# Kernel optimization log

Hardware: AMD Instinct MI355X
Metric: run time of the kernel (lower is better)

## Reference

```python
import jax, jax.numpy as jnp
import numpy as np

TOP_K = 6  # num_experts_per_tok


def setup_inputs() -> dict:
    key = jax.random.key(0)
    k1, k2, k3, k4, k5 = jax.random.split(key, 5)
    B, S, H = 2, 2048, 2048
    E, M = 28, 1408
    scale = 0.02
    return {
        "hidden_states": jax.random.normal(k1, (B, S, H), jnp.float32),
        "gate_weight": jax.random.normal(k2, (E, H), jnp.float32) * scale,
        "w_gate": jax.random.normal(k3, (E, H, M), jnp.float32) * scale,
        "w_up": jax.random.normal(k4, (E, H, M), jnp.float32) * scale,
        "w_down": jax.random.normal(k5, (E, M, H), jnp.float32) * scale,
    }


def reference(hidden_states, gate_weight, w_gate, w_up, w_down):
    """DeepseekMoE forward (inference path): top-k softmax gating + expert
    dispatch/combine. gate_weight: [E, H]; w_gate/w_up: [E, H, M]; w_down: [E, M, H]."""
    B, S, H = hidden_states.shape
    x = hidden_states.reshape(-1, H)          # [T, H]
    T = x.shape[0]
    E = gate_weight.shape[0]

    # --- MoEGate: softmax scores, top-k, normalize top-k probs ---
    logits = x @ gate_weight.T                # [T, E]
    scores = jax.nn.softmax(logits, axis=-1)
    topk_w, topk_idx = jax.lax.top_k(scores, TOP_K)  # [T, K]
    topk_w = topk_w / (topk_w.sum(axis=-1, keepdims=True) + 1e-20)

    # Dense per-(token, expert) combine weights (0 for non-selected experts).
    cw = jnp.zeros((T, E), x.dtype).at[jnp.arange(T)[:, None], topk_idx].add(topk_w)

    # --- Expert compute + combine, scanning over experts to bound memory ---
    def step(y, inp):
        wg, wu, wd, w_tok = inp               # [H,M], [H,M], [M,H], [T]
        h = jax.nn.silu(x @ wg) * (x @ wu)    # [T, M]
        return y + w_tok[:, None] * (h @ wd), None

    y0 = jnp.zeros_like(x)
    y, _ = jax.lax.scan(step, y0, (w_gate, w_up, w_down, cw.T))
    return y.reshape(B, S, H)
```

## Files before the change

### kernel.cpp

```cpp
#include <hip/hip_runtime.h>
#include <stdint.h>

#define T_TOK 4096
#define HDIM 2048
#define MDIM 1408
#define NEXP 28
#define TOPK 6
#define NPAIR (T_TOK*TOPK)

typedef unsigned short u16;
typedef short short8 __attribute__((ext_vector_type(8)));
typedef float f32x4 __attribute__((ext_vector_type(4)));

__device__ __forceinline__ u16 f2bf(float x){
  unsigned int u = __float_as_uint(x);
  u += 0x7fffu + ((u >> 16) & 1u);
  return (u16)(u >> 16);
}

__device__ __forceinline__ void gload16(const u16* g, u16* l){
  __builtin_amdgcn_global_load_lds((const __attribute__((address_space(1))) unsigned int*)g,
                                   (__attribute__((address_space(3))) unsigned int*)l,
                                   16, 0, 0);
}

__global__ __launch_bounds__(256) void cvt_kernel(const float* __restrict__ x,
                                                  u16* __restrict__ xb, int n8){
  int i = blockIdx.x*256 + threadIdx.x;
  if (i >= n8) return;
  const float4* s = (const float4*)x + (size_t)i*2;
  float4 a = s[0], b = s[1];
  unsigned int w0 = (unsigned)f2bf(a.x) | ((unsigned)f2bf(a.y)<<16);
  unsigned int w1 = (unsigned)f2bf(a.z) | ((unsigned)f2bf(a.w)<<16);
  unsigned int w2 = (unsigned)f2bf(b.x) | ((unsigned)f2bf(b.y)<<16);
  unsigned int w3 = (unsigned)f2bf(b.z) | ((unsigned)f2bf(b.w)<<16);
  uint4 o = {w0,w1,w2,w3};
  ((uint4*)xb)[i] = o;
}

__global__ __launch_bounds__(256) void transpose_cvt(const float* __restrict__ in,
                                                     u16* __restrict__ out, int K, int N){
  const int e = blockIdx.z;
  const int n0 = blockIdx.x*64, k0 = blockIdx.y*64;
  const float* src = in + ((size_t)e*K + k0)*N + n0;
  u16* dst = out + ((size_t)e*N + n0)*K + k0;
  __shared__ u16 td[64][65];
  const int tid = threadIdx.x;
  const int rk = tid>>4, rn = (tid&15)*4;
  #pragma unroll
  for (int i=0;i<4;i++){
    int k = rk + 16*i;
    float4 v = *(const float4*)(src + (size_t)k*N + rn);
    td[k][rn+0]=f2bf(v.x); td[k][rn+1]=f2bf(v.y);
    td[k][rn+2]=f2bf(v.z); td[k][rn+3]=f2bf(v.w);
  }
  __syncthreads();
  const int wn = tid>>4, wk = (tid&15)*4;
  #pragma unroll
  for (int i=0;i<4;i++){
    int n = wn + 16*i;
    unsigned int lo = (unsigned)td[wk+0][n] | ((unsigned)td[wk+1][n]<<16);
    unsigned int hi = (unsigned)td[wk+2][n] | ((unsigned)td[wk+3][n]<<16);
    uint2 o = {lo, hi};
    *(uint2*)(dst + (size_t)n*K + wk) = o;
  }
}

__global__ __launch_bounds__(256) void gate_kernel(const float* __restrict__ x,
                                                   const float* __restrict__ gw,
                                                   int* __restrict__ topk_idx,
                                                   float* __restrict__ topk_w,
                                                   int* __restrict__ counts){
  const int wave = threadIdx.x >> 6, lane = threadIdx.x & 63;
  const int t = blockIdx.x*4 + wave;
  const float* xr = x + (size_t)t*HDIM;
  float xv[32];
  #pragma unroll
  for (int i=0;i<32;i++) xv[i] = xr[lane + 64*i];
  float sc[NEXP];
  #pragma unroll
  for (int e=0;e<NEXP;e++){
    const float* g = gw + (size_t)e*HDIM + lane;
    float a = 0.f;
    #pragma unroll
    for (int i=0;i<32;i++) a += xv[i]*g[64*i];
    #pragma unroll
    for (int d=32; d>0; d>>=1) a += __shfl_xor(a, d);
    sc[e] = a;
  }
  float mx = sc[0];
  #pragma unroll
  for (int e=1;e<NEXP;e++) mx = fmaxf(mx, sc[e]);
  unsigned int mask=0; int bi[TOPK]; float bs[TOPK]; float bsum=0.f;
  #pragma unroll
  for (int k=0;k<TOPK;k++){
    float bm=-3.4e38f; int bj=0;
    #pragma unroll
    for (int e=0;e<NEXP;e++){
      bool ok = (((mask>>e)&1u)==0u) && (sc[e]>bm);
      bm = ok ? sc[e] : bm; bj = ok ? e : bj;
    }
    mask |= (1u<<bj);
    float s = expf(bm - mx);
    bi[k]=bj; bs[k]=s; bsum+=s;
  }
  if (lane==0){
    float inv = 1.f/(bsum + 1e-20f);
    #pragma unroll
    for (int k=0;k<TOPK;k++){
      topk_idx[t*TOPK+k]=bi[k];
      topk_w[t*TOPK+k]=bs[k]*inv;
      atomicAdd(&counts[bi[k]],1);
    }
  }
}

__global__ void scan_kernel(const int* __restrict__ counts, int* __restrict__ offsets,
                            int* __restrict__ cursor){
  int t = threadIdx.x;
  if (t < NEXP) cursor[t] = 0;
  if (t == 0){
    int s = 0;
    for (int e=0;e<NEXP;e++){ offsets[e]=s; s+=counts[e]; }
    offsets[NEXP]=s;
  }
}

__global__ __launch_bounds__(256) void fill_kernel(const int* __restrict__ topk_idx,
                                                   const float* __restrict__ topk_w,
                                                   const int* __restrict__ offsets,
                                                   int* __restrict__ cursor,
                                                   int* __restrict__ pair_token,
                                                   float* __restrict__ pair_w){
  int t = blockIdx.x*256 + threadIdx.x;
  if (t >= T_TOK) return;
  #pragma unroll
  for (int k=0;k<TOPK;k++){
    int e = topk_idx[t*TOPK+k];
    int pos = atomicAdd(&cursor[e],1);
    int p = offsets[e]+pos;
    pair_token[p]=t;
    pair_w[p]=topk_w[t*TOPK+k];
  }
}

template<int NB, bool GATHER, int EPI>
__global__ __launch_bounds__(256,2) void gemm2(
    const u16* __restrict__ Ab, const u16* __restrict__ B0, const u16* __restrict__ B1,
    u16* __restrict__ Hout, float* __restrict__ Out,
    const int* __restrict__ counts, const int* __restrict__ offsets,
    const int* __restrict__ pair_token, const float* __restrict__ pair_w,
    int K, int N)
{
  const int e = blockIdx.z;
  const int cnt = counts[e];
  const int row0 = blockIdx.y*128;
  if (row0 >= cnt) return;
  const int off = offsets[e];
  const int n0 = blockIdx.x*128;

  __shared__ u16 smem[(1+NB)*8192];

  const int tid = threadIdx.x;
  const int lane = tid&63, wid = tid>>6;
  const int wm = wid>>1, wn = wid&1;
  const int lrow = lane&15, lgrp = lane>>4;

  const u16* ap[4]; const u16* bp0[4]; const u16* bp1[4];
  #pragma unroll
  for (int i=0;i<4;i++){
    int c = tid + 256*i;
    int r = c>>3;
    int sc = (c&7) ^ (r&7);
    int pr = off + min(row0 + r, cnt-1);
    const u16* arow = GATHER ? (Ab + (size_t)pair_token[pr]*K) : (Ab + (size_t)pr*K);
    ap[i] = arow + sc*8;
    size_t brow = (size_t)e*N + (size_t)(n0 + r);
    bp0[i] = B0 + brow*K + sc*8;
    if (NB==2) bp1[i] = B1 + brow*K + sc*8;
  }

  int aoffs[2][4], boffs[2][4];
  #pragma unroll
  for (int kh=0;kh<2;kh++){
    #pragma unroll
    for (int f=0; f<4; f++){
      int mr = wm*64 + f*16 + lrow;
      aoffs[kh][f] = mr*64 + (((kh*4+lgrp) ^ (mr&7))*8);
      int nr = wn*64 + f*16 + lrow;
      boffs[kh][f] = nr*64 + (((kh*4+lgrp) ^ (nr&7))*8);
    }
  }

  f32x4 acc0[4][4] = {};
  f32x4 acc1[4][4] = {};

  for (int kt=0; kt<K; kt+=64){
    __syncthreads();
    #pragma unroll
    for (int i=0;i<4;i++){
      int ldo = (tid + 256*i)*8;
      gload16(ap[i] + kt, &smem[ldo]);
      gload16(bp0[i] + kt, &smem[8192 + ldo]);
      if (NB==2) gload16(bp1[i] + kt, &smem[16384 + ldo]);
    }
    __syncthreads();
    #pragma unroll
    for (int kh=0; kh<2; kh++){
      short8 af[4], b0f[4], b1f[4];
      #pragma unroll
      for (int f=0;f<4;f++){
        af[f]  = *(const short8*)&smem[aoffs[kh][f]];
        b0f[f] = *(const short8*)&smem[8192 + boffs[kh][f]];
        if (NB==2) b1f[f] = *(const short8*)&smem[16384 + boffs[kh][f]];
      }
      #pragma unroll
      for (int fm=0;fm<4;fm++){
        #pragma unroll
        for (int fn=0;fn<4;fn++){
          acc0[fm][fn] = __builtin_amdgcn_mfma_f32_16x16x32_bf16(af[fm], b0f[fn], acc0[fm][fn],0,0,0);
          if (NB==2)
            acc1[fm][fn] = __builtin_amdgcn_mfma_f32_16x16x32_bf16(af[fm], b1f[fn], acc1[fm][fn],0,0,0);
        }
      }
    }
  }

  #pragma unroll
  for (int fm=0;fm<4;fm++){
    #pragma unroll
    for (int j=0;j<4;j++){
      int grow = wm*64 + fm*16 + lgrp*4 + j;
      if (row0+grow < cnt){
        int p = off + row0 + grow;
        if (EPI==0){
          u16* hrow = Hout + (size_t)p*N;
          #pragma unroll
          for (int fn=0;fn<4;fn++){
            int col = n0 + wn*64 + fn*16 + lrow;
            float g = acc0[fm][fn][j], u = acc1[fm][fn][j];
            hrow[col] = f2bf(g*u/(1.f+expf(-g)));
          }
        } else {
          int tok = pair_token[p];
          float wgt = pair_w[p];
          float* orow = Out + (size_t)tok*N;
          #pragma unroll
          for (int fn=0;fn<4;fn++){
            int col = n0 + wn*64 + fn*16 + lrow;
            atomicAdd(orow + col, wgt*acc0[fm][fn][j]);
          }
        }
      }
    }
  }
}

extern "C" void kernel_launch(void* const* d_in, const int* in_sizes, int n_in,
                              void* d_out, int out_size, void* d_ws, size_t ws_size,
                              hipStream_t stream) {
  const float* x  = (const float*)d_in[0];
  const float* gw = (const float*)d_in[1];
  const float* wg = (const float*)d_in[2];
  const float* wu = (const float*)d_in[3];
  const float* wd = (const float*)d_in[4];
  float* out = (float*)d_out;

  const size_t WT_BYTES = (size_t)NEXP*MDIM*HDIM*2;

  char* p = (char*)d_ws;
  u16* wg_t = (u16*)p;
  u16* wd_t = (u16*)p;
  p += WT_BYTES;
  u16* wu_t = (u16*)p; p += WT_BYTES;
  u16* xb   = (u16*)p; p += (size_t)T_TOK*HDIM*2;
  u16* hbuf = (u16*)p; p += (size_t)NPAIR*MDIM*2;
  int*   topk_idx   = (int*)p;   p += NPAIR*4;
  float* topk_w     = (float*)p; p += NPAIR*4;
  int*   pair_token = (int*)p;   p += NPAIR*4;
  float* pair_w     = (float*)p; p += NPAIR*4;
  int*   counts     = (int*)p;   p += 128;
  int*   offsets    = (int*)p;   p += 128;
  int*   cursor     = (int*)p;   p += 128;

  hipMemsetAsync(counts, 0, 128, stream);
  cvt_kernel<<<T_TOK*HDIM/8/256, 256, 0, stream>>>(x, xb, T_TOK*HDIM/8);
  gate_kernel<<<T_TOK/4, 256, 0, stream>>>(x, gw, topk_idx, topk_w, counts);
  scan_kernel<<<1, 64, 0, stream>>>(counts, offsets, cursor);
  fill_kernel<<<T_TOK/256, 256, 0, stream>>>(topk_idx, topk_w, offsets, cursor, pair_token, pair_w);
  hipMemsetAsync(out, 0, (size_t)out_size*4, stream);

  transpose_cvt<<<dim3(MDIM/64, HDIM/64, NEXP), 256, 0, stream>>>(wg, wg_t, HDIM, MDIM);
  transpose_cvt<<<dim3(MDIM/64, HDIM/64, NEXP), 256, 0, stream>>>(wu, wu_t, HDIM, MDIM);

  gemm2<2,true,0><<<dim3(MDIM/128, T_TOK/128, NEXP), 256, 0, stream>>>(
      xb, wg_t, wu_t, hbuf, nullptr, counts, offsets, pair_token, pair_w, HDIM, MDIM);

  transpose_cvt<<<dim3(HDIM/64, MDIM/64, NEXP), 256, 0, stream>>>(wd, wd_t, MDIM, HDIM);

  gemm2<1,false,1><<<dim3(HDIM/128, T_TOK/128, NEXP), 256, 0, stream>>>(
      hbuf, wd_t, nullptr, nullptr, out, counts, offsets, pair_token, pair_w, MDIM, HDIM);
}
```

Baseline: 1.212 ms.

## Double-buffer MoE GEMM K-loop, replace atomic combine with gather kernel

Restructures the grouped expert GEMM to use BK=32 with double-buffered LDS, issuing the next tile's async global-to-LDS loads before waiting with explicit vmcnt, so memory latency overlaps MFMA work. The grid order is swapped so row tiles are the fastest-varying block index. The down-projection no longer does float atomicAdd into the output. It writes bf16 per-pair results, and a new combine kernel gathers the six pairs per token with their weights, which also drops the output memset. It also widens the transpose store to 16-byte writes with padded LDS. The costs are an extra bf16 rounding of the down-projection outputs and a second pass over a per-pair buffer.

Result: slower. 2.484 ms (+105.0%).

```diff
diff --git a/kernel.cpp b/kernel.cpp
--- a/kernel.cpp
+++ b/kernel.cpp
@@ -16,6 +16,9 @@
   unsigned int u = __float_as_uint(x);
   u += 0x7fffu + ((u >> 16) & 1u);
   return (u16)(u >> 16);
+}
+__device__ __forceinline__ float bf2f(unsigned int h){
+  return __uint_as_float(h << 16);
 }
 
 __device__ __forceinline__ void gload16(const u16* g, u16* l){
@@ -44,7 +47,7 @@
   const int n0 = blockIdx.x*64, k0 = blockIdx.y*64;
   const float* src = in + ((size_t)e*K + k0)*N + n0;
   u16* dst = out + ((size_t)e*N + n0)*K + k0;
-  __shared__ u16 td[64][65];
+  __shared__ u16 td[64][72];
   const int tid = threadIdx.x;
   const int rk = tid>>4, rn = (tid&15)*4;
   #pragma unroll
@@ -55,14 +58,16 @@
     td[k][rn+2]=f2bf(v.z); td[k][rn+3]=f2bf(v.w);
   }
   __syncthreads();
-  const int wn = tid>>4, wk = (tid&15)*4;
-  #pragma unroll
-  for (int i=0;i<4;i++){
-    int n = wn + 16*i;
-    unsigned int lo = (unsigned)td[wk+0][n] | ((unsigned)td[wk+1][n]<<16);
-    unsigned int hi = (unsigned)td[wk+2][n] | ((unsigned)td[wk+3][n]<<16);
-    uint2 o = {lo, hi};
-    *(uint2*)(dst + (size_t)n*K + wk) = o;
+  const int k8 = (tid&7)*8;
+  #pragma unroll
+  for (int i=0;i<2;i++){
+    int n = (tid>>3) + 32*i;
+    unsigned int w[4];
+    #pragma unroll
+    for (int j=0;j<4;j++)
+      w[j] = (unsigned)td[k8+2*j][n] | ((unsigned)td[k8+2*j+1][n]<<16);
+    uint4 o = {w[0],w[1],w[2],w[3]};
+    *(uint4*)(dst + (size_t)n*K + k8) = o;
   }
 }
 
@@ -131,99 +136,115 @@
                                                    const int* __restrict__ offsets,
                                                    int* __restrict__ cursor,
                                                    int* __restrict__ pair_token,
-                                                   float* __restrict__ pair_w){
+                                                   int* __restrict__ pos){
   int t = blockIdx.x*256 + threadIdx.x;
   if (t >= T_TOK) return;
   #pragma unroll
   for (int k=0;k<TOPK;k++){
     int e = topk_idx[t*TOPK+k];
-    int pos = atomicAdd(&cursor[e],1);
-    int p = offsets[e]+pos;
+    int c = atomicAdd(&cursor[e],1);
+    int p = offsets[e]+c;
     pair_token[p]=t;
-    pair_w[p]=topk_w[t*TOPK+k];
+    pos[t*TOPK+k]=p;
   }
 }
 
 template<int NB, bool GATHER, int EPI>
-__global__ __launch_bounds__(256,2) void gemm2(
+__global__ __launch_bounds__(256,2) void gemm3(
     const u16* __restrict__ Ab, const u16* __restrict__ B0, const u16* __restrict__ B1,
-    u16* __restrict__ Hout, float* __restrict__ Out,
+    u16* __restrict__ Hout,
     const int* __restrict__ counts, const int* __restrict__ offsets,
-    const int* __restrict__ pair_token, const float* __restrict__ pair_w,
+    const int* __restrict__ pair_token,
     int K, int N)
 {
   const int e = blockIdx.z;
   const int cnt = counts[e];
-  const int row0 = blockIdx.y*128;
+  const int row0 = blockIdx.x*128;
   if (row0 >= cnt) return;
   const int off = offsets[e];
-  const int n0 = blockIdx.x*128;
-
-  __shared__ u16 smem[(1+NB)*8192];
+  const int n0 = blockIdx.y*128;
+
+  __shared__ u16 smem[2*(1+NB)*4096];
 
   const int tid = threadIdx.x;
   const int lane = tid&63, wid = tid>>6;
   const int wm = wid>>1, wn = wid&1;
   const int lrow = lane&15, lgrp = lane>>4;
 
-  const u16* ap[4]; const u16* bp0[4]; const u16* bp1[4];
-  #pragma unroll
-  for (int i=0;i<4;i++){
-    int c = tid + 256*i;
-    int r = c>>3;
-    int sc = (c&7) ^ (r&7);
+  const u16* ap[2]; const u16* bp0[2]; const u16* bp1[2];
+  #pragma unroll
+  for (int j=0;j<2;j++){
+    int c = tid + 256*j;
+    int G = c>>3, s = c&7;
+    int u = s ^ (G&7);
+    int r = 2*G + (u>>2);
+    int g = u&3;
     int pr = off + min(row0 + r, cnt-1);
     const u16* arow = GATHER ? (Ab + (size_t)pair_token[pr]*K) : (Ab + (size_t)pr*K);
-    ap[i] = arow + sc*8;
+    ap[j] = arow + g*8;
     size_t brow = (size_t)e*N + (size_t)(n0 + r);
-    bp0[i] = B0 + brow*K + sc*8;
-    if (NB==2) bp1[i] = B1 + brow*K + sc*8;
-  }
-
-  int aoffs[2][4], boffs[2][4];
-  #pragma unroll
-  for (int kh=0;kh<2;kh++){
-    #pragma unroll
-    for (int f=0; f<4; f++){
-      int mr = wm*64 + f*16 + lrow;
-      aoffs[kh][f] = mr*64 + (((kh*4+lgrp) ^ (mr&7))*8);
-      int nr = wn*64 + f*16 + lrow;
-      boffs[kh][f] = nr*64 + (((kh*4+lgrp) ^ (nr&7))*8);
-    }
+    bp0[j] = B0 + brow*K + g*8;
+    if (NB==2) bp1[j] = B1 + brow*K + g*8;
+  }
+
+  int aoff[4], boff[4];
+  #pragma unroll
+  for (int f=0;f<4;f++){
+    int mr = wm*64 + f*16 + lrow;
+    aoff[f] = (mr>>1)*64 + (((((mr&1)<<2)|lgrp) ^ ((mr>>1)&7))*8);
+    int nr = wn*64 + f*16 + lrow;
+    boff[f] = (nr>>1)*64 + (((((nr&1)<<2)|lgrp) ^ ((nr>>1)&7))*8);
   }
 
   f32x4 acc0[4][4] = {};
   f32x4 acc1[4][4] = {};
 
-  for (int kt=0; kt<K; kt+=64){
-    __syncthreads();
-    #pragma unroll
-    for (int i=0;i<4;i++){
-      int ldo = (tid + 256*i)*8;
-      gload16(ap[i] + kt, &smem[ldo]);
-      gload16(bp0[i] + kt, &smem[8192 + ldo]);
-      if (NB==2) gload16(bp1[i] + kt, &smem[16384 + ldo]);
-    }
-    __syncthreads();
-    #pragma unroll
-    for (int kh=0; kh<2; kh++){
-      short8 af[4], b0f[4], b1f[4];
+  const int nt = K/32;
+  const int TB = (1+NB)*4096;
+  #pragma unroll
+  for (int j=0;j<2;j++){
+    int ldo = (tid + 256*j)*8;
+    gload16(ap[j], &smem[ldo]);
+    gload16(bp0[j], &smem[4096+ldo]);
+    if (NB==2) gload16(bp1[j], &smem[8192+ldo]);
+  }
+
+  for (int t=0; t<nt; ++t){
+    const int cur = (t&1)*TB;
+    const int nxt = ((t+1)&1)*TB;
+    if (t+1 < nt){
+      const int kt = (t+1)*32;
       #pragma unroll
-      for (int f=0;f<4;f++){
-        af[f]  = *(const short8*)&smem[aoffs[kh][f]];
-        b0f[f] = *(const short8*)&smem[8192 + boffs[kh][f]];
-        if (NB==2) b1f[f] = *(const short8*)&smem[16384 + boffs[kh][f]];
+      for (int j=0;j<2;j++){
+        int ldo = (tid + 256*j)*8;
+        gload16(ap[j] + kt, &smem[nxt + ldo]);
+        gload16(bp0[j] + kt, &smem[nxt + 4096 + ldo]);
+        if (NB==2) gload16(bp1[j] + kt, &smem[nxt + 8192 + ldo]);
       }
+      if (NB==2) asm volatile("s_waitcnt vmcnt(6)" ::: "memory");
+      else       asm volatile("s_waitcnt vmcnt(4)" ::: "memory");
+    } else {
+      asm volatile("s_waitcnt vmcnt(0)" ::: "memory");
+    }
+    __builtin_amdgcn_s_barrier();
+
+    short8 af[4], b0f[4], b1f[4];
+    #pragma unroll
+    for (int f=0;f<4;f++){
+      af[f]  = *(const short8*)&smem[cur + aoff[f]];
+      b0f[f] = *(const short8*)&smem[cur + 4096 + boff[f]];
+      if (NB==2) b1f[f] = *(const short8*)&smem[cur + 8192 + boff[f]];
+    }
+    #pragma unroll
+    for (int fm=0;fm<4;fm++){
       #pragma unroll
-      for (int fm=0;fm<4;fm++){
-        #pragma unroll
-        for (int fn=0;fn<4;fn++){
-          acc0[fm][fn] = __builtin_amdgcn_mfma_f32_16x16x32_bf16(af[fm], b0f[fn], acc0[fm][fn],0,0,0);
-          if (NB==2)
-            acc1[fm][fn] = __builtin_amdgcn_mfma_f32_16x16x32_bf16(af[fm], b1f[fn], acc1[fm][fn],0,0,0);
-        }
+      for (int fn=0;fn<4;fn++){
+        acc0[fm][fn] = __builtin_amdgcn_mfma_f32_16x16x32_bf16(af[fm], b0f[fn], acc0[fm][fn],0,0,0);
+        if (NB==2)
+          acc1[fm][fn] = __builtin_amdgcn_mfma_f32_16x16x32_bf16(af[fm], b1f[fn], acc1[fm][fn],0,0,0);
       }
     }
+    __builtin_amdgcn_s_barrier();
   }
 
   #pragma unroll
@@ -233,27 +254,46 @@
       int grow = wm*64 + fm*16 + lgrp*4 + j;
       if (row0+grow < cnt){
         int p = off + row0 + grow;
-        if (EPI==0){
-          u16* hrow = Hout + (size_t)p*N;
-          #pragma unroll
-          for (int fn=0;fn<4;fn++){
-            int col = n0 + wn*64 + fn*16 + lrow;
+        u16* hrow = Hout + (size_t)p*N;
+        #pragma unroll
+        for (int fn=0;fn<4;fn++){
+          int col = n0 + wn*64 + fn*16 + lrow;
+          if (EPI==0){
             float g = acc0[fm][fn][j], u = acc1[fm][fn][j];
             hrow[col] = f2bf(g*u/(1.f+expf(-g)));
-          }
-        } else {
-          int tok = pair_token[p];
-          float wgt = pair_w[p];
-          float* orow = Out + (size_t)tok*N;
-          #pragma unroll
-          for (int fn=0;fn<4;fn++){
-            int col = n0 + wn*64 + fn*16 + lrow;
-            atomicAdd(orow + col, wgt*acc0[fm][fn][j]);
+          } else {
+            hrow[col] = f2bf(acc0[fm][fn][j]);
           }
         }
       }
     }
   }
+}
+
+__global__ __launch_bounds__(256) void combine_kernel(const u16* __restrict__ pairbuf,
+                                                      const int* __restrict__ pos,
+                                                      const float* __restrict__ topk_w,
+                                                      float* __restrict__ out){
+  const int t = blockIdx.x;
+  const int c = threadIdx.x*8;
+  float acc[8] = {};
+  #pragma unroll
+  for (int k=0;k<TOPK;k++){
+    int p = pos[t*TOPK+k];
+    float w = topk_w[t*TOPK+k];
+    uint4 v = *(const uint4*)&pairbuf[(size_t)p*HDIM + c];
+    unsigned int ws_[4] = {v.x,v.y,v.z,v.w};
+    #pragma unroll
+    for (int j=0;j<4;j++){
+      acc[2*j]   += w*bf2f(ws_[j]&0xffffu);
+      acc[2*j+1] += w*bf2f(ws_[j]>>16);
+    }
+  }
+  float4 o0 = {acc[0],acc[1],acc[2],acc[3]};
+  float4 o1 = {acc[4],acc[5],acc[6],acc[7]};
+  float* orow = out + (size_t)t*HDIM + c;
+  *(float4*)orow = o0;
+  *(float4*)(orow+4) = o1;
 }
 
 extern "C" void kernel_launch(void* const* d_in, const int* in_sizes, int n_in,
@@ -272,13 +312,15 @@
   u16* wg_t = (u16*)p;
   u16* wd_t = (u16*)p;
   p += WT_BYTES;
-  u16* wu_t = (u16*)p; p += WT_BYTES;
+  u16* wu_t    = (u16*)p;
+  u16* pairbuf = (u16*)p;
+  p += WT_BYTES;
   u16* xb   = (u16*)p; p += (size_t)T_TOK*HDIM*2;
   u16* hbuf = (u16*)p; p += (size_t)NPAIR*MDIM*2;
   int*   topk_idx   = (int*)p;   p += NPAIR*4;
   float* topk_w     = (float*)p; p += NPAIR*4;
   int*   pair_token = (int*)p;   p += NPAIR*4;
-  float* pair_w     = (float*)p; p += NPAIR*4;
+  int*   pos        = (int*)p;   p += NPAIR*4;
   int*   counts     = (int*)p;   p += 128;
   int*   offsets    = (int*)p;   p += 128;
   int*   cursor     = (int*)p;   p += 128;
@@ -287,17 +329,18 @@
   cvt_kernel<<<T_TOK*HDIM/8/256, 256, 0, stream>>>(x, xb, T_TOK*HDIM/8);
   gate_kernel<<<T_TOK/4, 256, 0, stream>>>(x, gw, topk_idx, topk_w, counts);
   scan_kernel<<<1, 64, 0, stream>>>(counts, offsets, cursor);
-  fill_kernel<<<T_TOK/256, 256, 0, stream>>>(topk_idx, topk_w, offsets, cursor, pair_token, pair_w);
-  hipMemsetAsync(out, 0, (size_t)out_size*4, stream);
+  fill_kernel<<<T_TOK/256, 256, 0, stream>>>(topk_idx, topk_w, offsets, cursor, pair_token, pos);
 
   transpose_cvt<<<dim3(MDIM/64, HDIM/64, NEXP), 256, 0, stream>>>(wg, wg_t, HDIM, MDIM);
   transpose_cvt<<<dim3(MDIM/64, HDIM/64, NEXP), 256, 0, stream>>>(wu, wu_t, HDIM, MDIM);
 
-  gemm2<2,true,0><<<dim3(MDIM/128, T_TOK/128, NEXP), 256, 0, stream>>>(
-      xb, wg_t, wu_t, hbuf, nullptr, counts, offsets, pair_token, pair_w, HDIM, MDIM);
+  gemm3<2,true,0><<<dim3(32, MDIM/128, NEXP), 256, 0, stream>>>(
+      xb, wg_t, wu_t, hbuf, counts, offsets, pair_token, HDIM, MDIM);
 
   transpose_cvt<<<dim3(HDIM/64, MDIM/64, NEXP), 256, 0, stream>>>(wd, wd_t, MDIM, HDIM);
 
-  gemm2<1,false,1><<<dim3(HDIM/128, T_TOK/128, NEXP), 256, 0, stream>>>(
-      hbuf, wd_t, nullptr, nullptr, out, counts, offsets, pair_token, pair_w, MDIM, HDIM);
-}
+  gemm3<1,false,1><<<dim3(32, HDIM/128, NEXP), 256, 0, stream>>>(
+      hbuf, wd_t, nullptr, pairbuf, counts, offsets, pair_token, MDIM, HDIM);
+
+  combine_kernel<<<T_TOK, 256, 0, stream>>>(pairbuf, pos, topk_w, out);
+}
```
